# Performance work log

Measured on AMD Instinct MI355X. Metric: run time of the kernel, lower is better.

Reference implementation:

```python
import jax, jax.numpy as jnp
import numpy as np

B, T, D_MODEL = 4, 2048, 1024
D_EXPERT, N_EXPERTS, TOP_K = 4096, 8, 2
CAPACITY_FACTOR = 1.25
AUX_COEFF, Z_COEFF = 0.01, 0.001


def setup_inputs() -> dict:
    key = jax.random.key(0)
    k = jax.random.split(key, 4)
    x = jax.random.normal(k[0], (B, T, D_MODEL), jnp.float32)
    Wr = jax.random.normal(k[1], (D_MODEL, N_EXPERTS), jnp.float32) * 0.02
    W1 = jax.random.normal(k[2], (N_EXPERTS, D_MODEL, D_EXPERT), jnp.float32) * (1.0 / np.sqrt(D_MODEL))
    b1 = jnp.zeros((N_EXPERTS, D_EXPERT), jnp.float32)
    W2 = jax.random.normal(k[3], (N_EXPERTS, D_EXPERT, D_MODEL), jnp.float32) * (1.0 / np.sqrt(D_EXPERT))
    b2 = jnp.zeros((N_EXPERTS, D_MODEL), jnp.float32)
    return {"x": x, "Wr": Wr, "W1": W1, "b1": b1, "W2": W2, "b2": b2}


def reference(x, Wr, W1, b1, W2, b2):
    Bb, Tt, D = x.shape
    N = Bb * Tt
    E = W1.shape[0]
    capacity = max(1, int(N / E * CAPACITY_FACTOR * TOP_K))

    xf = x.reshape(N, D)
    logits = xf @ Wr                                    # (N, E)
    z_loss = jnp.mean(jax.nn.logsumexp(logits, axis=-1) ** 2)
    probs = jax.nn.softmax(logits, axis=-1)             # (N, E)

    topk_p, topk_i = jax.lax.top_k(probs, TOP_K)        # (N, K)
    # one-hot expert mask (top-k experts are distinct per token)
    mask = jnp.zeros((N, E), probs.dtype).at[jnp.arange(N)[:, None], topk_i].set(1.0)

    # capacity truncation: keep first `capacity` assigned tokens per expert, in token order
    pos = (jnp.cumsum(mask, axis=0) - mask).astype(jnp.int32)   # exclusive rank within expert
    keep = (pos < capacity) & (mask > 0)
    mask_t = jnp.where(keep, mask, jnp.zeros_like(mask))

    # Switch-style aux loss on truncated mask
    total_sel = jnp.maximum(mask_t.sum(), 1.0)
    f_i = mask_t.sum(axis=0) / total_sel
    P_i = probs.mean(axis=0)
    aux_loss = E * jnp.sum(f_i * P_i)

    # normalized top-k combine weights (differentiable through probs)
    tk_raw = jnp.take_along_axis(probs, topk_i, axis=1)          # (N, K)
    tk = tk_raw / jnp.maximum(tk_raw.sum(axis=-1, keepdims=True), 1e-9)

    # dispatch tokens into (E, capacity, D) buffer; dropped tokens scatter out of range
    pos_safe = jnp.where(keep, pos, capacity)                    # capacity -> dropped
    pos_k = jnp.take_along_axis(pos_safe, topk_i, axis=1)        # (N, K)
    upd = jnp.broadcast_to(xf[:, None, :], (N, TOP_K, D)).reshape(-1, D)
    buf = jnp.zeros((E, capacity, D), x.dtype).at[topk_i.reshape(-1), pos_k.reshape(-1)].set(upd, mode='drop')

    # grouped expert MLP
    h = jax.nn.relu(jnp.einsum('ecd,edf->ecf', buf, W1) + b1[:, None, :])
    eo = jnp.einsum('ecf,efd->ecd', h, W2) + b2[:, None, :]      # (E, capacity, D)

    # combine: gather each token's top-k expert outputs, weight, sum; dropped -> weight 0
    valid_k = jnp.take_along_axis(keep, topk_i, axis=1)          # (N, K) bool
    w = tk * valid_k.astype(tk.dtype)
    pos_g = jnp.minimum(pos_k, capacity - 1)
    gathered = eo[topk_i, pos_g]                                 # (N, K, D)
    out = jnp.einsum('nk,nkd->nd', w, gathered).reshape(Bb, Tt, D)

    total_aux = AUX_COEFF * aux_loss + Z_COEFF * z_loss
    return out, aux_loss, z_loss, total_aux
```

## Files before the change

### kernel.cpp

```cpp
#include <hip/hip_runtime.h>
#include <stdint.h>

#define N_TOK    8192
#define DM       1024
#define DE       4096
#define NEXP     8
#define CAP      2560
#define AUX_CO   0.01f
#define Z_CO     0.001f

typedef __attribute__((ext_vector_type(4))) float f32x4;
typedef __attribute__((ext_vector_type(8))) __bf16 bf16x8;

static __device__ __forceinline__ unsigned short f2bf(float f) {
  union { float f; uint32_t u; } v; v.f = f;
  uint32_t r = 0x7fffu + ((v.u >> 16) & 1u);
  return (unsigned short)((v.u + r) >> 16);
}
static __device__ __forceinline__ float bf2f(unsigned short u) {
  union { uint32_t u; float f; } v; v.u = ((uint32_t)u) << 16;
  return v.f;
}

#define MEMFENCE() asm volatile("" ::: "memory")
#define BAR()    do { MEMFENCE(); __builtin_amdgcn_s_barrier(); MEMFENCE(); } while (0)
#define LGKM0()  asm volatile("s_waitcnt lgkmcnt(0)" ::: "memory")
#define LGKM8()  asm volatile("s_waitcnt lgkmcnt(8)" ::: "memory")
#define VMW(N)   asm volatile("s_waitcnt vmcnt(" #N ")" ::: "memory")
#define SB0()    __builtin_amdgcn_sched_barrier(0)
#define GLD16(g, l) __builtin_amdgcn_global_load_lds( \
    (const __attribute__((address_space(1))) void*)(g), \
    (__attribute__((address_space(3))) void*)(l), 16, 0, 0)

__global__ __launch_bounds__(256) void transpose_to_bf16(
    const float* __restrict__ in, unsigned short* __restrict__ out, int R, int C)
{
  __shared__ float tile[32][33];
  const size_t eoff = (size_t)blockIdx.z * R * C;
  const int bx = blockIdx.x * 32, by = blockIdx.y * 32;
  const int r = threadIdx.x >> 3, c4 = (threadIdx.x & 7) * 4;
  const float4 v = *(const float4*)&in[eoff + (size_t)(by + r) * C + bx + c4];
  tile[r][c4 + 0] = v.x; tile[r][c4 + 1] = v.y;
  tile[r][c4 + 2] = v.z; tile[r][c4 + 3] = v.w;
  __syncthreads();
  const int oc = threadIdx.x >> 3, r4 = (threadIdx.x & 7) * 4;
  ushort4 o;
  o.x = f2bf(tile[r4 + 0][oc]); o.y = f2bf(tile[r4 + 1][oc]);
  o.z = f2bf(tile[r4 + 2][oc]); o.w = f2bf(tile[r4 + 3][oc]);
  *(ushort4*)&out[eoff + (size_t)(bx + oc) * R + by + r4] = o;
}

__global__ __launch_bounds__(256) void router_kernel(
    const float* __restrict__ x, const float* __restrict__ Wr,
    int* __restrict__ topk, float* __restrict__ tkw, float* __restrict__ zP)
{
  const int tid = threadIdx.x, lane = tid & 63, wave = tid >> 6;
  float zacc = 0.f;
  float pacc[NEXP];
#pragma unroll
  for (int e = 0; e < NEXP; ++e) pacc[e] = 0.f;

  for (int it = 0; it < 4; ++it) {
    const int t = blockIdx.x * 16 + it * 4 + wave;
    float acc[NEXP];
#pragma unroll
    for (int e = 0; e < NEXP; ++e) acc[e] = 0.f;
    const f32x4* x4 = (const f32x4*)(x + (size_t)t * DM);
#pragma unroll
    for (int i = 0; i < 4; ++i) {
      f32x4 xv = x4[i * 64 + lane];
#pragma unroll
      for (int j = 0; j < 4; ++j) {
        const float xs = xv[j];
        const float* wr = Wr + (size_t)((i * 64 + lane) * 4 + j) * NEXP;
#pragma unroll
        for (int e = 0; e < NEXP; ++e) acc[e] += xs * wr[e];
      }
    }
#pragma unroll
    for (int m = 32; m; m >>= 1)
#pragma unroll
      for (int e = 0; e < NEXP; ++e) acc[e] += __shfl_xor(acc[e], m);

    float mx = acc[0];
#pragma unroll
    for (int e = 1; e < NEXP; ++e) mx = fmaxf(mx, acc[e]);
    float p[NEXP], s = 0.f;
#pragma unroll
    for (int e = 0; e < NEXP; ++e) { p[e] = expf(acc[e] - mx); s += p[e]; }
    const float lse = mx + logf(s);
    zacc += lse * lse;
    const float inv_s = 1.f / s;
#pragma unroll
    for (int e = 0; e < NEXP; ++e) pacc[e] += p[e] * inv_s;

    int e0 = 0; float v0 = p[0];
#pragma unroll
    for (int e = 1; e < NEXP; ++e) if (p[e] > v0) { v0 = p[e]; e0 = e; }
    int e1 = -1; float v1 = -1.f;
#pragma unroll
    for (int e = 0; e < NEXP; ++e) if (e != e0 && p[e] > v1) { v1 = p[e]; e1 = e; }

    const float pr0 = v0 * inv_s, pr1 = v1 * inv_s;
    const float denom = fmaxf(pr0 + pr1, 1e-9f);
    if (lane == 0) {
      topk[2*t]   = e0; topk[2*t+1] = e1;
      tkw[2*t]    = pr0 / denom; tkw[2*t+1] = pr1 / denom;
    }
  }
  __shared__ float blk[4][9];
  if (lane == 0) {
    blk[wave][0] = zacc;
#pragma unroll
    for (int e = 0; e < NEXP; ++e) blk[wave][1 + e] = pacc[e];
  }
  __syncthreads();
  if (tid < 9)
    zP[blockIdx.x * 9 + tid] = blk[0][tid] + blk[1][tid] + blk[2][tid] + blk[3][tid];
}

__global__ __launch_bounds__(512) void scan_kernel(
    const int2* __restrict__ topk, const float2* __restrict__ tkw,
    int* __restrict__ posk, float* __restrict__ wts,
    int* __restrict__ inv, int* __restrict__ kept)
{
  __shared__ int2   stopk[N_TOK];
  __shared__ float2 stkw[N_TOK];
  const int tid = threadIdx.x;
  for (int j = tid; j < N_TOK; j += 512) { stopk[j] = topk[j]; stkw[j] = tkw[j]; }
  __syncthreads();

  const int lane = tid & 63;
  const int e = tid >> 6;
  int base = 0;
  const uint64_t below = (lane == 63) ? 0xFFFFFFFFFFFFFFFFull >> 1
                                      : ((1ull << lane) - 1ull);
  for (int i = 0; i < N_TOK / 64; ++i) {
    const int t = i * 64 + lane;
    const int2 ti = stopk[t];
    const float2 w = stkw[t];
    const bool hit = (ti.x == e) || (ti.y == e);
    const uint64_t m = __ballot(hit);
    if (hit) {
      const int pos = base + (int)__popcll(m & below);
      const bool kp = pos < CAP;
      const int k = (ti.x == e) ? 0 : 1;
      posk[2*t + k] = kp ? pos : CAP;
      wts[2*t + k]  = kp ? ((k == 0) ? w.x : w.y) : 0.f;
      if (kp) inv[e * CAP + pos] = t;
    }
    base += (int)__popcll(m);
  }
  const int tail = base < CAP ? base : CAP;
  for (int q = tail + lane; q < CAP; q += 64) inv[e * CAP + q] = -1;
  if (lane == 0) kept[e] = tail;
}

__global__ __launch_bounds__(256) void dispatch_kernel(
    const float* __restrict__ x, const int* __restrict__ inv,
    unsigned short* __restrict__ buf)
{
  const int slot = blockIdx.x;
  const int t = inv[slot];
  ushort4 o;
  if (t >= 0) {
    const f32x4 v = ((const f32x4*)(x + (size_t)t * DM))[threadIdx.x];
    o.x = f2bf(v[0]); o.y = f2bf(v[1]); o.z = f2bf(v[2]); o.w = f2bf(v[3]);
  } else {
    o.x = 0; o.y = 0; o.z = 0; o.w = 0;
  }
  ((ushort4*)(buf + (size_t)slot * DM))[threadIdx.x] = o;
}

template<int BM, int BN, bool RELU>
__global__ __launch_bounds__(512, (BM == 256) ? 2 : 4) void gemm2p(
    const unsigned short* __restrict__ A,
    const unsigned short* __restrict__ Bt,
    const float* __restrict__ bias,
    unsigned short* __restrict__ C,
    const int* __restrict__ kept,
    int M, int N, int K, int mt, int nt, int nwg)
{
  constexpr int MF = BM / 32;
  constexpr int NF = BN / 64;
  constexpr int ABUF = BM * 64;
  constexpr int BBUF = BN * 64;
  __shared__ __attribute__((aligned(16))) unsigned short As[2 * ABUF];
  __shared__ __attribute__((aligned(16))) unsigned short Bs[2 * BBUF];

  const int tid = threadIdx.x, lane = tid & 63, wave = tid >> 6;
  const int wr = wave >> 2, wc = wave & 3;
  const int frow = lane & 15, kgrp = lane >> 4;

  int wg = (int)blockIdx.x;
  wg = (wg & 7) * (nwg >> 3) + (wg >> 3);
  const int ntpe = mt * nt;
  const int e = wg / ntpe, rr = wg % ntpe;
  const int m0 = (rr / nt) * BM;
  const int n0 = (rr % nt) * BN;
  if (m0 >= kept[e]) return;

  const unsigned short* Ae = A  + (size_t)e * M * K + (size_t)m0 * K;
  const unsigned short* Be = Bt + (size_t)e * N * K + (size_t)n0 * K;

  const int srow = tid >> 3;
  const int scol = ((tid & 7) ^ (srow & 7)) * 8;

  auto stage = [&](int buf, int k0) {
#pragma unroll
    for (int i = 0; i < BM / 64; ++i)
      GLD16(Ae + (size_t)(i * 64 + srow) * K + (k0 + scol),
            &As[buf * ABUF + i * 4096 + tid * 8]);
#pragma unroll
    for (int i = 0; i < BN / 64; ++i)
      GLD16(Be + (size_t)(i * 64 + srow) * K + (k0 + scol),
            &Bs[buf * BBUF + i * 4096 + tid * 8]);
  };

  f32x4 acc[MF][NF];
#pragma unroll
  for (int m = 0; m < MF; ++m)
#pragma unroll
    for (int n = 0; n < NF; ++n) acc[m][n] = (f32x4){0.f, 0.f, 0.f, 0.f};

  const int nk = K >> 6;
  stage(0, 0);
  for (int t = 0; t < nk; ++t) {
    const int cur = t & 1;
    __syncthreads();
    if (t + 1 < nk) stage(cur ^ 1, (t + 1) * 64);
#pragma unroll
    for (int kk = 0; kk < 2; ++kk) {
      bf16x8 bq[NF], af[MF];
#pragma unroll
      for (int n = 0; n < NF; ++n) {
        const int row = wc * (BN / 4) + n * 16 + frow;
        const int slot = (kk * 4 + kgrp) ^ (row & 7);
        bq[n] = *(const bf16x8*)&Bs[cur * BBUF + row * 64 + slot * 8];
      }
#pragma unroll
      for (int m = 0; m < MF; ++m) {
        const int row = wr * (BM / 2) + m * 16 + frow;
        const int slot = (kk * 4 + kgrp) ^ (row & 7);
        af[m] = *(const bf16x8*)&As[cur * ABUF + row * 64 + slot * 8];
      }
      __builtin_amdgcn_s_setprio(1);
#pragma unroll
      for (int m = 0; m < MF; ++m)
#pragma unroll
        for (int n = 0; n < NF; ++n)
          acc[m][n] = __builtin_amdgcn_mfma_f32_16x16x32_bf16(af[m], bq[n], acc[m][n], 0, 0, 0);
      __builtin_amdgcn_s_setprio(0);
    }
  }

  const int r0 = m0 + wr * (BM / 2) + 4 * kgrp;
  const int c0 = n0 + wc * (BN / 4) + frow;
#pragma unroll
  for (int n = 0; n < NF; ++n) {
    const int cc = c0 + n * 16;
    const float bv = bias[(size_t)e * N + cc];
#pragma unroll
    for (int m = 0; m < MF; ++m) {
#pragma unroll
      for (int r = 0; r < 4; ++r) {
        float v = acc[m][n][r] + bv;
        if (RELU) v = fmaxf(v, 0.f);
        C[((size_t)e * M + (r0 + m * 16 + r)) * N + cc] = f2bf(v);
      }
    }
  }
}

template<bool RELU>
__global__ __launch_bounds__(512, 2) void gemm8p(
    const unsigned short* __restrict__ A,
    const unsigned short* __restrict__ Bt,
    const float* __restrict__ bias,
    unsigned short* __restrict__ C,
    const int* __restrict__ kept,
    int M, int N, int K, int mt, int nt, int nwg)
{
  __shared__ __attribute__((aligned(16))) unsigned short As[2 * 16384];
  __shared__ __attribute__((aligned(16))) unsigned short Bs[2 * 16384];
  const int tid = threadIdx.x, lane = tid & 63, wave = tid >> 6;
  const int wr = wave >> 2, wc = wave & 3;
  const int frow = lane & 15, kgrp = lane >> 4;

  int wg = (int)blockIdx.x;
  wg = (wg & 7) * (nwg >> 3) + (wg >> 3);
  const int ntpe = mt * nt;
  const int e = wg / ntpe, rr = wg % ntpe;
  const int m0 = (rr / nt) * 256;
  const int n0 = (rr % nt) * 256;
  if (m0 >= kept[e]) return;

  const unsigned short* Ae = A  + (size_t)e * M * K + (size_t)m0 * K;
  const unsigned short* Be = Bt + (size_t)e * N * K + (size_t)n0 * K;

  const int srow = tid >> 3;
  const int scol = ((tid & 7) ^ (srow & 7)) * 8;

  auto stA = [&](int t, int h) {
    const int c = t & 1, k0 = t * 64;
#pragma unroll
    for (int i = 0; i < 2; ++i)
      GLD16(Ae + (size_t)(h * 128 + i * 64 + srow) * K + (k0 + scol),
            &As[c * 16384 + (h * 128 + i * 64) * 64 + tid * 8]);
  };
  auto stB = [&](int t, int h) {
    const int c = t & 1, k0 = t * 64;
#pragma unroll
    for (int i = 0; i < 2; ++i)
      GLD16(Be + (size_t)(h * 128 + i * 64 + srow) * K + (k0 + scol),
            &Bs[c * 16384 + (h * 128 + i * 64) * 64 + tid * 8]);
  };
  auto rdA = [&](bf16x8* dst, int c, int mh) {
#pragma unroll
    for (int m = 0; m < 4; ++m) {
      const int row = wr * 128 + mh * 64 + m * 16 + frow;
#pragma unroll
      for (int kk = 0; kk < 2; ++kk)
        dst[m * 2 + kk] = *(const bf16x8*)
          &As[c * 16384 + row * 64 + (((kk * 4 + kgrp) ^ (row & 7)) * 8)];
    }
  };
  auto rdB = [&](bf16x8* dst, int c, int nh) {
#pragma unroll
    for (int n = 0; n < 2; ++n) {
      const int row = wc * 64 + nh * 32 + n * 16 + frow;
#pragma unroll
      for (int kk = 0; kk < 2; ++kk)
        dst[n * 2 + kk] = *(const bf16x8*)
          &Bs[c * 16384 + row * 64 + (((kk * 4 + kgrp) ^ (row & 7)) * 8)];
    }
  };

  f32x4 acc[8][4];
#pragma unroll
  for (int m = 0; m < 8; ++m)
#pragma unroll
    for (int n = 0; n < 4; ++n) acc[m][n] = (f32x4){0.f, 0.f, 0.f, 0.f};

  bf16x8 af0[8], af1[8], bq0[4], bq1[4];
  auto mfmaQ = [&](int mh, int nh, bf16x8* af, bf16x8* bq) {
#pragma unroll
    for (int m = 0; m < 4; ++m)
#pragma unroll
      for (int n = 0; n < 2; ++n)
#pragma unroll
        for (int kk = 0; kk < 2; ++kk)
          acc[mh * 4 + m][nh * 2 + n] = __builtin_amdgcn_mfma_f32_16x16x32_bf16(
              af[m * 2 + kk], bq[n * 2 + kk], acc[mh * 4 + m][nh * 2 + n], 0, 0, 0);
  };

  const int nk = K >> 6;

  stA(0, 0); stA(0, 1); stB(0, 0); stB(0, 1);
  stA(1, 0); stA(1, 1); stB(1, 0);
  VMW(6);
  BAR();

  for (int t = 0; t < nk; ++t) {
    const int c = t & 1;
    rdA(af0, c, 0);
    rdB(bq0, c, 0);
    if (t + 1 < nk) stB(t + 1, 1);
    LGKM8();
    BAR(); LGKM0(); SB0();
    __builtin_amdgcn_s_setprio(1);
    mfmaQ(0, 0, af0, bq0);
    __builtin_amdgcn_s_setprio(0);
    BAR();
    rdA(af1, c, 1);
    BAR(); LGKM0(); SB0();
    __builtin_amdgcn_s_setprio(1);
    mfmaQ(1, 0, af1, bq0);
    __builtin_amdgcn_s_setprio(0);
    BAR();
    rdB(bq1, c, 1);
    if (t + 2 < nk) stA(t + 2, 0);
    BAR(); LGKM0(); SB0();
    __builtin_amdgcn_s_setprio(1);
    mfmaQ(0, 1, af0, bq1);
    __builtin_amdgcn_s_setprio(0);
    BAR();
    if (t + 2 < nk) { stA(t + 2, 1); stB(t + 2, 0); }
    BAR(); SB0();
    __builtin_amdgcn_s_setprio(1);
    mfmaQ(1, 1, af1, bq1);
    __builtin_amdgcn_s_setprio(0);
    if (t + 2 < nk)      { VMW(6); }
    else if (t + 1 < nk) { VMW(0); }
    if (t + 1 < nk) BAR();
  }

  const int r0 = m0 + wr * 128 + 4 * kgrp;
  const int c0 = n0 + wc * 64 + frow;
#pragma unroll
  for (int nf = 0; nf < 4; ++nf) {
    const int cc = c0 + nf * 16;
    const float bv = bias[(size_t)e * N + cc];
#pragma unroll
    for (int m = 0; m < 8; ++m) {
#pragma unroll
      for (int r = 0; r < 4; ++r) {
        float v = acc[m][nf][r] + bv;
        if (RELU) v = fmaxf(v, 0.f);
        C[((size_t)e * M + (r0 + m * 16 + r)) * N + cc] = f2bf(v);
      }
    }
  }
}

__global__ __launch_bounds__(256) void combine_kernel(
    const unsigned short* __restrict__ eo, const int* __restrict__ posk,
    const float* __restrict__ wts, const int* __restrict__ topk,
    float* __restrict__ out)
{
  const int t = blockIdx.x;
  const int e0 = topk[2*t], e1 = topk[2*t+1];
  int p0 = posk[2*t], p1 = posk[2*t+1];
  p0 = p0 < CAP - 1 ? p0 : CAP - 1;
  p1 = p1 < CAP - 1 ? p1 : CAP - 1;
  const float w0 = wts[2*t], w1 = wts[2*t+1];
  const ushort4 a = ((const ushort4*)(eo + ((size_t)e0 * CAP + p0) * DM))[threadIdx.x];
  const ushort4 b = ((const ushort4*)(eo + ((size_t)e1 * CAP + p1) * DM))[threadIdx.x];
  f32x4 o;
  o[0] = w0 * bf2f(a.x) + w1 * bf2f(b.x);
  o[1] = w0 * bf2f(a.y) + w1 * bf2f(b.y);
  o[2] = w0 * bf2f(a.z) + w1 * bf2f(b.z);
  o[3] = w0 * bf2f(a.w) + w1 * bf2f(b.w);
  ((f32x4*)(out + (size_t)t * DM))[threadIdx.x] = o;
}

__global__ __launch_bounds__(64) void finalize_kernel(
    const float* __restrict__ zP, const int* __restrict__ kept,
    float* __restrict__ outs)
{
  const int lane = threadIdx.x;
  float v[9];
#pragma unroll
  for (int e = 0; e < 9; ++e) {
    float s = 0.f;
    for (int b = 0; b < 8; ++b) s += zP[(lane * 8 + b) * 9 + e];
    v[e] = s;
  }
#pragma unroll
  for (int m = 32; m; m >>= 1)
#pragma unroll
    for (int e = 0; e < 9; ++e) v[e] += __shfl_xor(v[e], m);
  if (lane == 0) {
    const float z = v[0] / (float)N_TOK;
    float total = 0.f;
    for (int e = 0; e < NEXP; ++e) total += (float)kept[e];
    total = fmaxf(total, 1.f);
    float aux = 0.f;
    for (int e = 0; e < NEXP; ++e)
      aux += ((float)kept[e] / total) * (v[1 + e] / (float)N_TOK);
    aux *= (float)NEXP;
    outs[0] = aux;
    outs[1] = z;
    outs[2] = AUX_CO * aux + Z_CO * z;
  }
}

extern "C" void kernel_launch(void* const* d_in, const int* in_sizes, int n_in,
                              void* d_out, int out_size, void* d_ws, size_t ws_size,
                              hipStream_t stream)
{
  const float* x  = (const float*)d_in[0];
  const float* Wr = (const float*)d_in[1];
  const float* W1 = (const float*)d_in[2];
  const float* b1 = (const float*)d_in[3];
  const float* W2 = (const float*)d_in[4];
  const float* b2 = (const float*)d_in[5];
  float* out = (float*)d_out;

  char* p = (char*)d_ws;
  auto alloc = [&](size_t bytes) {
    char* q = p; p += (bytes + 255) & ~(size_t)255; return q;
  };
  unsigned short* W1t = (unsigned short*)alloc((size_t)NEXP * DM * DE * 2);
  unsigned short* W2t = (unsigned short*)alloc((size_t)NEXP * DM * DE * 2);
  unsigned short* buf = (unsigned short*)alloc((size_t)NEXP * CAP * DM * 2);
  unsigned short* h   = (unsigned short*)alloc((size_t)NEXP * CAP * DE * 2);
  unsigned short* eo  = (unsigned short*)alloc((size_t)NEXP * CAP * DM * 2);
  int*   topk = (int*)alloc((size_t)N_TOK * 2 * 4);
  float* tkw  = (float*)alloc((size_t)N_TOK * 2 * 4);
  int*   posk = (int*)alloc((size_t)N_TOK * 2 * 4);
  float* wts  = (float*)alloc((size_t)N_TOK * 2 * 4);
  int*   inv  = (int*)alloc((size_t)NEXP * CAP * 4);
  int*   kept = (int*)alloc((size_t)NEXP * 4);
  float* zP   = (float*)alloc((size_t)512 * 9 * 4);

  transpose_to_bf16<<<dim3(DE / 32, DM / 32, NEXP), 256, 0, stream>>>(W1, W1t, DM, DE);
  transpose_to_bf16<<<dim3(DM / 32, DE / 32, NEXP), 256, 0, stream>>>(W2, W2t, DE, DM);
  router_kernel<<<512, 256, 0, stream>>>(x, Wr, topk, tkw, zP);
  scan_kernel<<<1, 512, 0, stream>>>((const int2*)topk, (const float2*)tkw, posk, wts, inv, kept);
  dispatch_kernel<<<NEXP * CAP, 256, 0, stream>>>(x, inv, buf);

  gemm8p<true><<<1280, 512, 0, stream>>>(buf, W1t, b1, h, kept, CAP, DE, DM, 10, 16, 1280);
  gemm2p<128, 128, false><<<1280, 512, 0, stream>>>(
      h, W2t, b2, eo, kept, CAP, DM, DE, 20, 8, 1280);

  combine_kernel<<<N_TOK, 256, 0, stream>>>(eo, posk, wts, topk, out);
  finalize_kernel<<<1, 64, 0, stream>>>(zP, kept, out + (size_t)N_TOK * DM);
}
```

Baseline: 592.7 us.

## Replace second expert GEMM with 320x128 pipelined kernel, widen transpose, fuse finalize

The second expert GEMM moves from a 128x128 double-buffered kernel to a new 320x128-tile kernel. It stages A two k-steps ahead and interleaves LDS reads, global-to-LDS loads and MFMA quarters with explicit barriers and waitcnts, which cuts the grid to 512 workgroups and raises reuse of A and B per tile. The weight transpose now uses 64x64 tiles with 16-byte bf16 stores, reducing launch count and giving wider writes. The finalize kernel is folded into the combine kernel to save one launch. The larger tile lowers occupancy and launches fewer workgroups, which may leave CUs underused.

```diff
diff --git a/kernel.cpp b/kernel.cpp
--- a/kernel.cpp
+++ b/kernel.cpp
@@ -35,19 +35,28 @@
 __global__ __launch_bounds__(256) void transpose_to_bf16(
     const float* __restrict__ in, unsigned short* __restrict__ out, int R, int C)
 {
-  __shared__ float tile[32][33];
+  __shared__ float tile[64][65];
   const size_t eoff = (size_t)blockIdx.z * R * C;
-  const int bx = blockIdx.x * 32, by = blockIdx.y * 32;
-  const int r = threadIdx.x >> 3, c4 = (threadIdx.x & 7) * 4;
-  const float4 v = *(const float4*)&in[eoff + (size_t)(by + r) * C + bx + c4];
-  tile[r][c4 + 0] = v.x; tile[r][c4 + 1] = v.y;
-  tile[r][c4 + 2] = v.z; tile[r][c4 + 3] = v.w;
+  const int bx = blockIdx.x * 64, by = blockIdx.y * 64;
+  const int r = threadIdx.x >> 2, c16 = (threadIdx.x & 3) * 16;
+#pragma unroll
+  for (int j = 0; j < 4; ++j) {
+    const float4 v = *(const float4*)&in[eoff + (size_t)(by + r) * C + bx + c16 + j * 4];
+    tile[r][c16 + j * 4 + 0] = v.x; tile[r][c16 + j * 4 + 1] = v.y;
+    tile[r][c16 + j * 4 + 2] = v.z; tile[r][c16 + j * 4 + 3] = v.w;
+  }
   __syncthreads();
-  const int oc = threadIdx.x >> 3, r4 = (threadIdx.x & 7) * 4;
-  ushort4 o;
-  o.x = f2bf(tile[r4 + 0][oc]); o.y = f2bf(tile[r4 + 1][oc]);
-  o.z = f2bf(tile[r4 + 2][oc]); o.w = f2bf(tile[r4 + 3][oc]);
-  *(ushort4*)&out[eoff + (size_t)(bx + oc) * R + by + r4] = o;
+  const int oc = threadIdx.x >> 2, r16 = (threadIdx.x & 3) * 16;
+#pragma unroll
+  for (int half = 0; half < 2; ++half) {
+    uint4 o;
+    const int rb = r16 + half * 8;
+    o.x = (uint32_t)f2bf(tile[rb + 0][oc]) | ((uint32_t)f2bf(tile[rb + 1][oc]) << 16);
+    o.y = (uint32_t)f2bf(tile[rb + 2][oc]) | ((uint32_t)f2bf(tile[rb + 3][oc]) << 16);
+    o.z = (uint32_t)f2bf(tile[rb + 4][oc]) | ((uint32_t)f2bf(tile[rb + 5][oc]) << 16);
+    o.w = (uint32_t)f2bf(tile[rb + 6][oc]) | ((uint32_t)f2bf(tile[rb + 7][oc]) << 16);
+    *(uint4*)&out[eoff + (size_t)(bx + oc) * R + by + rb] = o;
+  }
 }
 
 __global__ __launch_bounds__(256) void router_kernel(
@@ -172,106 +181,6 @@
   ((ushort4*)(buf + (size_t)slot * DM))[threadIdx.x] = o;
 }
 
-template<int BM, int BN, bool RELU>
-__global__ __launch_bounds__(512, (BM == 256) ? 2 : 4) void gemm2p(
-    const unsigned short* __restrict__ A,
-    const unsigned short* __restrict__ Bt,
-    const float* __restrict__ bias,
-    unsigned short* __restrict__ C,
-    const int* __restrict__ kept,
-    int M, int N, int K, int mt, int nt, int nwg)
-{
-  constexpr int MF = BM / 32;
-  constexpr int NF = BN / 64;
-  constexpr int ABUF = BM * 64;
-  constexpr int BBUF = BN * 64;
-  __shared__ __attribute__((aligned(16))) unsigned short As[2 * ABUF];
-  __shared__ __attribute__((aligned(16))) unsigned short Bs[2 * BBUF];
-
-  const int tid = threadIdx.x, lane = tid & 63, wave = tid >> 6;
-  const int wr = wave >> 2, wc = wave & 3;
-  const int frow = lane & 15, kgrp = lane >> 4;
-
-  int wg = (int)blockIdx.x;
-  wg = (wg & 7) * (nwg >> 3) + (wg >> 3);
-  const int ntpe = mt * nt;
-  const int e = wg / ntpe, rr = wg % ntpe;
-  const int m0 = (rr / nt) * BM;
-  const int n0 = (rr % nt) * BN;
-  if (m0 >= kept[e]) return;
-
-  const unsigned short* Ae = A  + (size_t)e * M * K + (size_t)m0 * K;
-  const unsigned short* Be = Bt + (size_t)e * N * K + (size_t)n0 * K;
-
-  const int srow = tid >> 3;
-  const int scol = ((tid & 7) ^ (srow & 7)) * 8;
-
-  auto stage = [&](int buf, int k0) {
-#pragma unroll
-    for (int i = 0; i < BM / 64; ++i)
-      GLD16(Ae + (size_t)(i * 64 + srow) * K + (k0 + scol),
-            &As[buf * ABUF + i * 4096 + tid * 8]);
-#pragma unroll
-    for (int i = 0; i < BN / 64; ++i)
-      GLD16(Be + (size_t)(i * 64 + srow) * K + (k0 + scol),
-            &Bs[buf * BBUF + i * 4096 + tid * 8]);
-  };
-
-  f32x4 acc[MF][NF];
-#pragma unroll
-  for (int m = 0; m < MF; ++m)
-#pragma unroll
-    for (int n = 0; n < NF; ++n) acc[m][n] = (f32x4){0.f, 0.f, 0.f, 0.f};
-
-  const int nk = K >> 6;
-  stage(0, 0);
-  for (int t = 0; t < nk; ++t) {
-    const int cur = t & 1;
-    __syncthreads();
-    if (t + 1 < nk) stage(cur ^ 1, (t + 1) * 64);
-#pragma unroll
-    for (int kk = 0; kk < 2; ++kk) {
-      bf16x8 bq[NF], af[MF];
-#pragma unroll
-      for (int n = 0; n < NF; ++n) {
-        const int row = wc * (BN / 4) + n * 16 + frow;
-        const int slot = (kk * 4 + kgrp) ^ (row & 7);
-        bq[n] = *(const bf16x8*)&Bs[cur * BBUF + row * 64 + slot * 8];
-      }
-#pragma unroll
-      for (int m = 0; m < MF; ++m) {
-        const int row = wr * (BM / 2) + m * 16 + frow;
-        const int slot = (kk * 4 + kgrp) ^ (row & 7);
-        af[m] = *(const bf16x8*)&As[cur * ABUF + row * 64 + slot * 8];
-      }
-      __builtin_amdgcn_s_setprio(1);
-#pragma unroll
-      for (int m = 0; m < MF; ++m)
-#pragma unroll
-        for (int n = 0; n < NF; ++n)
-          acc[m][n] = __builtin_amdgcn_mfma_f32_16x16x32_bf16(af[m], bq[n], acc[m][n], 0, 0, 0);
-      __builtin_amdgcn_s_setprio(0);
-    }
-  }
-
-  const int r0 = m0 + wr * (BM / 2) + 4 * kgrp;
-  const int c0 = n0 + wc * (BN / 4) + frow;
-#pragma unroll
-  for (int n = 0; n < NF; ++n) {
-    const int cc = c0 + n * 16;
-    const float bv = bias[(size_t)e * N + cc];
-#pragma unroll
-    for (int m = 0; m < MF; ++m) {
-#pragma unroll
-      for (int r = 0; r < 4; ++r) {
-        float v = acc[m][n][r] + bv;
-        if (RELU) v = fmaxf(v, 0.f);
-        C[((size_t)e * M + (r0 + m * 16 + r)) * N + cc] = f2bf(v);
-      }
-    }
-  }
-}
-
 template<bool RELU>
 __global__ __launch_bounds__(512, 2) void gemm8p(
     const unsigned short* __restrict__ A,
@@ -413,10 +322,146 @@
   }
 }
 
+template<bool RELU>
+__global__ __launch_bounds__(512, 2) void gemm8w(
+    const unsigned short* __restrict__ A,
+    const unsigned short* __restrict__ Bt,
+    const float* __restrict__ bias,
+    unsigned short* __restrict__ C,
+    const int* __restrict__ kept,
+    int M, int N, int K, int mt, int nt, int nwg)
+{
+  __shared__ __attribute__((aligned(16))) unsigned short As[2 * 20480];
+  __shared__ __attribute__((aligned(16))) unsigned short Bs[2 * 8192];
+  const int tid = threadIdx.x, lane = tid & 63, wave = tid >> 6;
+  const int wr = wave >> 2, wc = wave & 3;
+  const int frow = lane & 15, kgrp = lane >> 4;
+
+  int wg = (int)blockIdx.x;
+  wg = (wg & 7) * (nwg >> 3) + (wg >> 3);
+  const int ntpe = mt * nt;
+  const int e = wg / ntpe, rr = wg % ntpe;
+  const int m0 = (rr / nt) * 320;
+  const int n0 = (rr % nt) * 128;
+  if (m0 >= kept[e]) return;
+
+  const unsigned short* Ae = A  + (size_t)e * M * K + (size_t)m0 * K;
+  const unsigned short* Be = Bt + (size_t)e * N * K + (size_t)n0 * K;
+
+  const int srow = tid >> 3;
+  const int scol = ((tid & 7) ^ (srow & 7)) * 8;
+
+  auto stA = [&](int t, int g) {
+    const int c = t & 1, k0 = t * 64;
+    GLD16(Ae + (size_t)(g * 64 + srow) * K + (k0 + scol),
+          &As[c * 20480 + g * 4096 + tid * 8]);
+  };
+  auto stB = [&](int t) {
+    const int c = t & 1, k0 = t * 64;
+#pragma unroll
+    for (int i = 0; i < 2; ++i)
+      GLD16(Be + (size_t)(i * 64 + srow) * K + (k0 + scol),
+            &Bs[c * 8192 + i * 4096 + tid * 8]);
+  };
+  auto rdA = [&](bf16x8* dst, int c, int mh) {
+#pragma unroll
+    for (int m = 0; m < 5; ++m) {
+      const int row = wr * 160 + mh * 80 + m * 16 + frow;
+#pragma unroll
+      for (int kk = 0; kk < 2; ++kk)
+        dst[m * 2 + kk] = *(const bf16x8*)
+          &As[c * 20480 + row * 64 + (((kk * 4 + kgrp) ^ (row & 7)) * 8)];
+    }
+  };
+  auto rdB = [&](bf16x8* dst, int c, int nh) {
+    const int row = wc * 32 + nh * 16 + frow;
+#pragma unroll
+    for (int kk = 0; kk < 2; ++kk)
+      dst[kk] = *(const bf16x8*)
+        &Bs[c * 8192 + row * 64 + (((kk * 4 + kgrp) ^ (row & 7)) * 8)];
+  };
+
+  f32x4 acc[10][2];
+#pragma unroll
+  for (int m = 0; m < 10; ++m)
+#pragma unroll
+    for (int n = 0; n < 2; ++n) acc[m][n] = (f32x4){0.f, 0.f, 0.f, 0.f};
+
+  bf16x8 af[10], bq0[2], bq1[2];
+  auto mfmaQ = [&](int mh, int nh, bf16x8* bq) {
+#pragma unroll
+    for (int m = 0; m < 5; ++m)
+#pragma unroll
+      for (int kk = 0; kk < 2; ++kk)
+        acc[mh * 5 + m][nh] = __builtin_amdgcn_mfma_f32_16x16x32_bf16(
+            af[m * 2 + kk], bq[kk], acc[mh * 5 + m][nh], 0, 0, 0);
+  };
+
+  const int nk = K >> 6;
+
+  stA(0, 0); stA(0, 1); stA(0, 2); stA(0, 3); stA(0, 4);
+  stB(0);
+  stA(1, 0); stA(1, 1); stA(1, 2); stA(1, 3); stA(1, 4);
+  VMW(5);
+  BAR();
+
+  for (int t = 0; t < nk; ++t) {
+    const int c = t & 1;
+    rdA(af, c, 0);
+    rdB(bq0, c, 0);
+    if (t + 1 < nk) stB(t + 1);
+    LGKM8();
+    BAR(); LGKM0(); SB0();
+    __builtin_amdgcn_s_setprio(1);
+    mfmaQ(0, 0, bq0);
+    __builtin_amdgcn_s_setprio(0);
+    BAR();
+    rdB(bq1, c, 1);
+    if (t + 2 < nk) stA(t + 2, 0);
+    BAR(); LGKM0(); SB0();
+    __builtin_amdgcn_s_setprio(1);
+    mfmaQ(0, 1, bq1);
+    __builtin_amdgcn_s_setprio(0);
+    BAR();
+    rdA(af, c, 1);
+    BAR(); LGKM0(); SB0();
+    __builtin_amdgcn_s_setprio(1);
+    mfmaQ(1, 0, bq0);
+    __builtin_amdgcn_s_setprio(0);
+    BAR();
+    if (t + 2 < nk) { stA(t + 2, 1); stA(t + 2, 2); stA(t + 2, 3); stA(t + 2, 4); }
+    BAR(); SB0();
+    __builtin_amdgcn_s_setprio(1);
+    mfmaQ(1, 1, bq1);
+    __builtin_amdgcn_s_setprio(0);
+    if (t + 2 < nk)      { VMW(5); }
+    else if (t + 1 < nk) { VMW(0); }
+    if (t + 1 < nk) BAR();
+  }
+
+  const int r0 = m0 + wr * 160 + 4 * kgrp;
+  const int c0 = n0 + wc * 32 + frow;
+#pragma unroll
+  for (int nf = 0; nf < 2; ++nf) {
+    const int cc = c0 + nf * 16;
+    const float bv = bias[(size_t)e * N + cc];
+#pragma unroll
+    for (int m = 0; m < 10; ++m) {
+#pragma unroll
+      for (int r = 0; r < 4; ++r) {
+        float v = acc[m][nf][r] + bv;
+        if (RELU) v = fmaxf(v, 0.f);
+        C[((size_t)e * M + (r0 + m * 16 + r)) * N + cc] = f2bf(v);
+      }
+    }
+  }
+}
+
 __global__ __launch_bounds__(256) void combine_kernel(
     const unsigned short* __restrict__ eo, const int* __restrict__ posk,
     const float* __restrict__ wts, const int* __restrict__ topk,
-    float* __restrict__ out)
+    const float* __restrict__ zP, const int* __restrict__ kept,
+    float* __restrict__ out, float* __restrict__ outs)
 {
   const int t = blockIdx.x;
   const int e0 = topk[2*t], e1 = topk[2*t+1];
@@ -432,36 +477,33 @@
   o[2] = w0 * bf2f(a.z) + w1 * bf2f(b.z);
   o[3] = w0 * bf2f(a.w) + w1 * bf2f(b.w);
   ((f32x4*)(out + (size_t)t * DM))[threadIdx.x] = o;
-}
-
-__global__ __launch_bounds__(64) void finalize_kernel(
-    const float* __restrict__ zP, const int* __restrict__ kept,
-    float* __restrict__ outs)
-{
-  const int lane = threadIdx.x;
-  float v[9];
-#pragma unroll
-  for (int e = 0; e < 9; ++e) {
-    float s = 0.f;
-    for (int b = 0; b < 8; ++b) s += zP[(lane * 8 + b) * 9 + e];
-    v[e] = s;
-  }
-#pragma unroll
-  for (int m = 32; m; m >>= 1)
-#pragma unroll
-    for (int e = 0; e < 9; ++e) v[e] += __shfl_xor(v[e], m);
-  if (lane == 0) {
-    const float z = v[0] / (float)N_TOK;
-    float total = 0.f;
-    for (int e = 0; e < NEXP; ++e) total += (float)kept[e];
-    total = fmaxf(total, 1.f);
-    float aux = 0.f;
-    for (int e = 0; e < NEXP; ++e)
-      aux += ((float)kept[e] / total) * (v[1 + e] / (float)N_TOK);
-    aux *= (float)NEXP;
-    outs[0] = aux;
-    outs[1] = z;
-    outs[2] = AUX_CO * aux + Z_CO * z;
+
+  if (t == 0 && threadIdx.x < 64) {
+    const int lane = threadIdx.x;
+    float v[9];
+#pragma unroll
+    for (int e = 0; e < 9; ++e) {
+      float s = 0.f;
+      for (int bk = 0; bk < 8; ++bk) s += zP[(lane * 8 + bk) * 9 + e];
+      v[e] = s;
+    }
+#pragma unroll
+    for (int m = 32; m; m >>= 1)
+#pragma unroll
+      for (int e = 0; e < 9; ++e) v[e] += __shfl_xor(v[e], m);
+    if (lane == 0) {
+      const float z = v[0] / (float)N_TOK;
+      float total = 0.f;
+      for (int e = 0; e < NEXP; ++e) total += (float)kept[e];
+      total = fmaxf(total, 1.f);
+      float aux = 0.f;
+      for (int e = 0; e < NEXP; ++e)
+        aux += ((float)kept[e] / total) * (v[1 + e] / (float)N_TOK);
+      aux *= (float)NEXP;
+      outs[0] = aux;
+      outs[1] = z;
+      outs[2] = AUX_CO * aux + Z_CO * z;
+    }
   }
 }
 
@@ -494,16 +536,15 @@
   int*   kept = (int*)alloc((size_t)NEXP * 4);
   float* zP   = (float*)alloc((size_t)512 * 9 * 4);
 
-  transpose_to_bf16<<<dim3(DE / 32, DM / 32, NEXP), 256, 0, stream>>>(W1, W1t, DM, DE);
-  transpose_to_bf16<<<dim3(DM / 32, DE / 32, NEXP), 256, 0, stream>>>(W2, W2t, DE, DM);
+  transpose_to_bf16<<<dim3(DE / 64, DM / 64, NEXP), 256, 0, stream>>>(W1, W1t, DM, DE);
+  transpose_to_bf16<<<dim3(DM / 64, DE / 64, NEXP), 256, 0, stream>>>(W2, W2t, DE, DM);
   router_kernel<<<512, 256, 0, stream>>>(x, Wr, topk, tkw, zP);
   scan_kernel<<<1, 512, 0, stream>>>((const int2*)topk, (const float2*)tkw, posk, wts, inv, kept);
   dispatch_kernel<<<NEXP * CAP, 256, 0, stream>>>(x, inv, buf);
 
   gemm8p<true><<<1280, 512, 0, stream>>>(buf, W1t, b1, h, kept, CAP, DE, DM, 10, 16, 1280);
-  gemm2p<128, 128, false><<<1280, 512, 0, stream>>>(
-      h, W2t, b2, eo, kept, CAP, DM, DE, 20, 8, 1280);
-
-  combine_kernel<<<N_TOK, 256, 0, stream>>>(eo, posk, wts, topk, out);
-  finalize_kernel<<<1, 64, 0, stream>>>(zP, kept, out + (size_t)N_TOK * DM);
-}
+  gemm8w<false><<<512, 512, 0, stream>>>(h, W2t, b2, eo, kept, CAP, DM, DE, 8, 8, 512);
+
+  combine_kernel<<<N_TOK, 256, 0, stream>>>(eo, posk, wts, topk, zP, kept,
+                                            out, out + (size_t)N_TOK * DM);
+}
```

After: 636.4 us. +7.4%, slower.
